# Kernel optimization log

Hardware: AMD Instinct MI355X
Metric: run time of the kernel (lower is better)

The kernel has to match this reference:

```python
import jax, jax.numpy as jnp
import numpy as np

D_MODEL = 1024
NUM_HEADS = 16
HEAD_DIM = D_MODEL // NUM_HEADS


def setup_inputs() -> dict:
    key = jax.random.key(0)
    ks = jax.random.split(key, 5)
    x = jax.random.normal(ks[0], (2, 2048, D_MODEL), dtype=jnp.float32)
    # torch nn.Linear init scale ~ U(-1/sqrt(in), 1/sqrt(in)); use small normals
    s = 1.0 / np.sqrt(D_MODEL)
    W_qkv = jax.random.normal(ks[1], (D_MODEL, 3 * D_MODEL), dtype=jnp.float32) * s
    b_qkv = jax.random.normal(ks[2], (3 * D_MODEL,), dtype=jnp.float32) * s
    W_out = jax.random.normal(ks[3], (D_MODEL, D_MODEL), dtype=jnp.float32) * s
    b_out = jax.random.normal(ks[4], (D_MODEL,), dtype=jnp.float32) * s
    return {"x": x, "W_qkv": W_qkv, "b_qkv": b_qkv, "W_out": W_out, "b_out": b_out}


def reference(x, W_qkv, b_qkv, W_out, b_out):
    B, S, _ = x.shape
    qkv = x @ W_qkv + b_qkv                                  # [B,S,3D]
    qkv = qkv.reshape(B, S, NUM_HEADS, 3 * HEAD_DIM).transpose(0, 2, 1, 3)  # [B,H,S,3d]
    q, k, v = jnp.split(qkv, 3, axis=-1)                     # each [B,H,S,d]
    scale = 1.0 / np.sqrt(HEAD_DIM)
    scores = jnp.einsum("bhqd,bhkd->bhqk", q, k) * scale      # [B,H,S,S]
    attn = jax.nn.softmax(scores, axis=-1)
    values = jnp.einsum("bhqk,bhkd->bhqd", attn, v)           # [B,H,S,d]
    values = values.transpose(0, 2, 1, 3).reshape(B, S, D_MODEL)
    return values @ W_out + b_out
```

## Files before the change

### kernel.cpp

```cpp
#include <hip/hip_runtime.h>


#define D_MODEL 1024
#define NHEAD   16
#define HDIM    64
#define SEQ     2048
#define BATCH   2
#define NTOK    (BATCH * SEQ)

typedef float    f32x4  __attribute__((ext_vector_type(4)));
typedef float    f32x16 __attribute__((ext_vector_type(16)));
typedef _Float16 f16x8  __attribute__((ext_vector_type(8)));
typedef _Float16 f16x4  __attribute__((ext_vector_type(4)));

#define GLOBAL_LOAD_LDS16(gptr, lptr)                                            \
    __builtin_amdgcn_global_load_lds(                                            \
        (const __attribute__((address_space(1))) unsigned int*)(gptr),           \
        (__attribute__((address_space(3))) unsigned int*)(lptr), 16, 0, 0)

__global__ __launch_bounds__(256) void prep_kernel(
    const float* __restrict__ x, _Float16* __restrict__ xh,
    const float* __restrict__ Wqkv, _Float16* __restrict__ wq_t,
    const float* __restrict__ Wout, _Float16* __restrict__ wo_t)
{
    const int bx = blockIdx.x;
    const int tid = threadIdx.x;
    if (bx < 4096) {
        const int i = (bx * 256 + tid) * 4;
        const float4 v = *(const float4*)&x[i];
        f16x4 hh;
        hh[0] = (_Float16)v.x; hh[1] = (_Float16)v.y;
        hh[2] = (_Float16)v.z; hh[3] = (_Float16)v.w;
        *(f16x4*)&xh[i] = hh;
        return;
    }
    __shared__ float ts[64][65];
    const float* W; _Float16* Wt; int N, n0, k0;
    if (bx < 4096 + 768) {
        const int local = bx - 4096;
        W = Wqkv; Wt = wq_t; N = 3072;
        n0 = (local % 48) * 64; k0 = (local / 48) * 64;
    } else {
        const int local = bx - 4864;
        W = Wout; Wt = wo_t; N = 1024;
        n0 = (local % 16) * 64; k0 = (local / 16) * 64;
    }
    {
        const int r = tid >> 2, c = (tid & 3) << 4;
        const float* src = W + (size_t)(k0 + r) * N + n0 + c;
        #pragma unroll
        for (int u = 0; u < 4; ++u)
            *(float4*)&ts[r][c + u * 4] = *(const float4*)&src[u * 4];
    }
    __syncthreads();
    {
        const int n = tid >> 2, kg = (tid & 3) << 4;
        f16x8 v0, v1;
        #pragma unroll
        for (int j = 0; j < 8; ++j) {
            v0[j] = (_Float16)ts[kg + j][n];
            v1[j] = (_Float16)ts[kg + 8 + j][n];
        }
        _Float16* dst = Wt + (size_t)(n0 + n) * D_MODEL + k0 + kg;
        *(f16x8*)&dst[0] = v0;
        *(f16x8*)&dst[8] = v1;
    }
}

__global__ __launch_bounds__(512) void gemm_qkv_kernel(
    const _Float16* __restrict__ A, const _Float16* __restrict__ Bt,
    const float* __restrict__ bias, _Float16* __restrict__ Cout,
    int M, int N, int K)
{
    __shared__ _Float16 lds[2][4096];
    const int tid = threadIdx.x;
    const int wave = tid >> 6, lane = tid & 63;
    const int quad = lane >> 4, l16 = lane & 15;
    const int m0 = blockIdx.y * 128, n0 = blockIdx.x * 128;
    const int wr = wave >> 1, wc = wave & 1;

    f32x4 acc[2][4] = {};

    const bool isA = wave < 4;
    const _Float16* gsrc = isA ? (A + (size_t)m0 * K) : (Bt + (size_t)n0 * K);
    _Float16* ldst = isA ? &lds[0][0] : &lds[1][0];
    const int sbase = (wave & 3) * 2;

    for (int k0 = 0; k0 < K; k0 += 32) {
        __syncthreads();
        #pragma unroll
        for (int j = 0; j < 2; ++j) {
            const int seg = sbase + j;
            const int chunk = seg >> 1;
            const int row = ((seg & 1) << 6) | lane;
            GLOBAL_LOAD_LDS16(gsrc + (size_t)row * K + k0 + chunk * 8, ldst + seg * 512);
        }
        __syncthreads();

        f16x8 a[2], b[4];
        #pragma unroll
        for (int mt = 0; mt < 2; ++mt)
            a[mt] = *(const f16x8*)&lds[0][quad * 1024 + (wr * 32 + mt * 16 + l16) * 8];
        #pragma unroll
        for (int nt = 0; nt < 4; ++nt)
            b[nt] = *(const f16x8*)&lds[1][quad * 1024 + (wc * 64 + nt * 16 + l16) * 8];
        #pragma unroll
        for (int mt = 0; mt < 2; ++mt)
            #pragma unroll
            for (int nt = 0; nt < 4; ++nt)
                acc[mt][nt] = __builtin_amdgcn_mfma_f32_16x16x32_f16(a[mt], b[nt], acc[mt][nt], 0, 0, 0);
    }

    #pragma unroll
    for (int nt = 0; nt < 4; ++nt) {
        const int col = n0 + wc * 64 + nt * 16 + l16;
        const float bv = bias[col];
        #pragma unroll
        for (int mt = 0; mt < 2; ++mt) {
            #pragma unroll
            for (int r = 0; r < 4; ++r) {
                const int row = m0 + wr * 32 + mt * 16 + quad * 4 + r;
                Cout[(size_t)row * N + col] = (_Float16)(acc[mt][nt][r] + bv);
            }
        }
    }
}

__global__ __launch_bounds__(512) void gemm_out_kernel(
    const _Float16* __restrict__ A, const _Float16* __restrict__ Bt,
    const float* __restrict__ bias, float* __restrict__ Cout)
{
    const int K = D_MODEL, N = D_MODEL;
    __shared__ _Float16 ldsA[4096];
    __shared__ _Float16 ldsB[2048];
    const int tid = threadIdx.x;
    const int wave = tid >> 6, lane = tid & 63;
    const int quad = lane >> 4, l16 = lane & 15;
    const int m0 = blockIdx.y * 128, n0 = blockIdx.x * 64;
    const int wr = wave >> 1, wc = wave & 1;

    f32x4 acc[2][2] = {};

    for (int k0 = 0; k0 < K; k0 += 32) {
        __syncthreads();
        if (wave < 4) {
            #pragma unroll
            for (int j = 0; j < 2; ++j) {
                const int seg = wave * 2 + j;
                const int chunk = seg >> 1;
                const int row = ((seg & 1) << 6) | lane;
                GLOBAL_LOAD_LDS16(A + (size_t)(m0 + row) * K + k0 + chunk * 8, ldsA + seg * 512);
            }
        } else {
            const int seg = wave - 4;
            GLOBAL_LOAD_LDS16(Bt + (size_t)(n0 + lane) * K + k0 + seg * 8, ldsB + seg * 512);
        }
        __syncthreads();

        f16x8 a[2], b[2];
        #pragma unroll
        for (int mt = 0; mt < 2; ++mt)
            a[mt] = *(const f16x8*)&ldsA[quad * 1024 + (wr * 32 + mt * 16 + l16) * 8];
        #pragma unroll
        for (int nt = 0; nt < 2; ++nt)
            b[nt] = *(const f16x8*)&ldsB[quad * 512 + (wc * 32 + nt * 16 + l16) * 8];
        #pragma unroll
        for (int mt = 0; mt < 2; ++mt)
            #pragma unroll
            for (int nt = 0; nt < 2; ++nt)
                acc[mt][nt] = __builtin_amdgcn_mfma_f32_16x16x32_f16(a[mt], b[nt], acc[mt][nt], 0, 0, 0);
    }

    #pragma unroll
    for (int nt = 0; nt < 2; ++nt) {
        const int col = n0 + wc * 32 + nt * 16 + l16;
        const float bv = bias[col];
        #pragma unroll
        for (int mt = 0; mt < 2; ++mt) {
            #pragma unroll
            for (int r = 0; r < 4; ++r) {
                const int row = m0 + wr * 32 + mt * 16 + quad * 4 + r;
                Cout[(size_t)row * N + col] = acc[mt][nt][r] + bv;
            }
        }
    }
}

__global__ __launch_bounds__(256) void swizzle_kv_kernel(
    const _Float16* __restrict__ qkv,
    _Float16* __restrict__ Ksw, _Float16* __restrict__ Vsw)
{
    __shared__ _Float16 ts[64][72];
    const int tid = threadIdx.x;
    const int s0 = blockIdx.x * 64, h = blockIdx.y, b = blockIdx.z;
    const size_t hsz = (size_t)8 * SEQ * 8;
    _Float16* kh = Ksw + (size_t)(b * NHEAD + h) * hsz;
    _Float16* vh = Vsw + (size_t)(b * NHEAD + h) * hsz;

    {
        const int s = s0 + (tid >> 2);
        const int dg = (tid & 3) << 4;
        const _Float16* src = qkv + (size_t)(b * SEQ + s) * (3 * D_MODEL) + h * (3 * HDIM) + HDIM + dg;
        const f16x8 v0 = *(const f16x8*)&src[0];
        const f16x8 v1 = *(const f16x8*)&src[8];
        const int c0 = dg >> 3;
        *(f16x8*)&kh[((size_t)c0 * SEQ + s) * 8]       = v0;
        *(f16x8*)&kh[((size_t)(c0 + 1) * SEQ + s) * 8] = v1;
    }
    {
        const int s = tid >> 2, dg = (tid & 3) << 4;
        const _Float16* src = qkv + (size_t)(b * SEQ + s0 + s) * (3 * D_MODEL) + h * (3 * HDIM) + 2 * HDIM + dg;
        *(f16x8*)&ts[s][dg]     = *(const f16x8*)&src[0];
        *(f16x8*)&ts[s][dg + 8] = *(const f16x8*)&src[8];
    }
    __syncthreads();
    {
        const int d = tid >> 2, sg = (tid & 3) << 4;
        f16x8 v0, v1;
        #pragma unroll
        for (int j = 0; j < 8; ++j) { v0[j] = ts[sg + j][d]; v1[j] = ts[sg + 8 + j][d]; }
        const int cs0 = (s0 + sg) >> 3;
        *(f16x8*)&vh[((size_t)cs0 * HDIM + d) * 8]       = v0;
        *(f16x8*)&vh[((size_t)(cs0 + 1) * HDIM + d) * 8] = v1;
    }
}

__device__ __forceinline__ void softmax_frag(
    const f32x16 s0, const f32x16 s1, float& rs, f16x8 pa[4])
{
    #pragma unroll
    for (int half = 0; half < 2; ++half) {
        const f32x16 sv = half ? s1 : s0;
        float p[16];
        #pragma unroll
        for (int r = 0; r < 16; ++r)
            p[r] = __builtin_amdgcn_exp2f(sv[r]);
        #pragma unroll
        for (int r = 0; r < 16; r += 4)
            rs += (p[r] + p[r + 1]) + (p[r + 2] + p[r + 3]);

        union { f16x8 hv; unsigned u[4]; } lo, hh;
        {
            const unsigned A = __builtin_bit_cast(unsigned, __builtin_amdgcn_cvt_pkrtz(p[0], p[1]));
            const unsigned B = __builtin_bit_cast(unsigned, __builtin_amdgcn_cvt_pkrtz(p[2], p[3]));
            const unsigned C = __builtin_bit_cast(unsigned, __builtin_amdgcn_cvt_pkrtz(p[4], p[5]));
            const unsigned D = __builtin_bit_cast(unsigned, __builtin_amdgcn_cvt_pkrtz(p[6], p[7]));
            const auto rac = __builtin_amdgcn_permlane32_swap(A, C, false, false);
            const auto rbd = __builtin_amdgcn_permlane32_swap(B, D, false, false);
            lo.u[0] = rac[0]; lo.u[1] = rbd[0]; lo.u[2] = rac[1]; lo.u[3] = rbd[1];
        }
        {
            const unsigned E = __builtin_bit_cast(unsigned, __builtin_amdgcn_cvt_pkrtz(p[8],  p[9]));
            const unsigned F = __builtin_bit_cast(unsigned, __builtin_amdgcn_cvt_pkrtz(p[10], p[11]));
            const unsigned G = __builtin_bit_cast(unsigned, __builtin_amdgcn_cvt_pkrtz(p[12], p[13]));
            const unsigned H = __builtin_bit_cast(unsigned, __builtin_amdgcn_cvt_pkrtz(p[14], p[15]));
            const auto reg = __builtin_amdgcn_permlane32_swap(E, G, false, false);
            const auto rfh = __builtin_amdgcn_permlane32_swap(F, H, false, false);
            hh.u[0] = reg[0]; hh.u[1] = rfh[0]; hh.u[2] = reg[1]; hh.u[3] = rfh[1];
        }
        pa[half * 2]     = lo.hv;
        pa[half * 2 + 1] = hh.hv;
    }
}

__global__ __launch_bounds__(512) void attn_mfma_kernel(
    const _Float16* __restrict__ qkv,
    const _Float16* __restrict__ Ksw, const _Float16* __restrict__ Vsw,
    _Float16* __restrict__ val)
{
    __shared__ _Float16 Ks[2][8192];
    __shared__ _Float16 Vts[2][8192];

    const int tid = threadIdx.x;
    const int wave = tid >> 6, lane = tid & 63;
    const int l31 = lane & 31, hi = lane >> 5;

    const int id = blockIdx.x;
    const int g  = (id & 7) * 32 + (id >> 3);
    const int qt = g & 7, hb = g >> 3;
    const int h  = hb & 15, b = hb >> 4;
    const int q0 = qt * 256;

    const size_t hsz = (size_t)8 * SEQ * 8;
    const _Float16* kh = Ksw + (size_t)(b * NHEAD + h) * hsz;
    const _Float16* vh = Vsw + (size_t)(b * NHEAD + h) * hsz;

    f16x8 qf[4];
    {
        const int row = q0 + wave * 32 + l31;
        const _Float16* src = qkv + (size_t)(b * SEQ + row) * (3 * D_MODEL) + h * (3 * HDIM) + hi * 8;
        #pragma unroll
        for (int kk = 0; kk < 4; ++kk) {
            const f16x8 t = *(const f16x8*)(src + kk * 16);
            #pragma unroll
            for (int j = 0; j < 8; ++j)
                qf[kk][j] = (_Float16)((float)t[j] * 0.1803368802f);
        }
    }

    f32x16 acc0 = {};
    f32x16 acc1 = {};
    float rs = 0.f;

    const int sidx0 = wave * 2;
    #pragma unroll
    for (int j = 0; j < 2; ++j) {
        const int idx = sidx0 + j;
        const int u = idx >> 3, c = idx & 7;
        GLOBAL_LOAD_LDS16(kh + ((size_t)c * SEQ + u * 64 + lane) * 8, &Ks[0][idx * 512]);
        GLOBAL_LOAD_LDS16(vh + ((size_t)(u * 8 + c) * HDIM + lane) * 8, &Vts[0][idx * 512]);
    }
    __syncthreads();

    for (int kt = 0; kt < SEQ / 128; ++kt) {
        const int cur = kt & 1;

        if (kt + 1 < SEQ / 128) {
            #pragma unroll
            for (int j = 0; j < 2; ++j) {
                const int idx = sidx0 + j;
                const int u = idx >> 3, c = idx & 7;
                GLOBAL_LOAD_LDS16(kh + ((size_t)c * SEQ + (kt + 1) * 128 + u * 64 + lane) * 8,
                                  &Ks[cur ^ 1][idx * 512]);
                GLOBAL_LOAD_LDS16(vh + ((size_t)((kt + 1) * 16 + u * 8 + c) * HDIM + lane) * 8,
                                  &Vts[cur ^ 1][idx * 512]);
            }
        }

        #pragma unroll
        for (int u = 0; u < 2; ++u) {
            const _Float16* ksub = &Ks[cur][u * 4096];
            const _Float16* vsub = &Vts[cur][u * 4096];

            f32x16 s0 = {}, s1 = {};
            __builtin_amdgcn_s_setprio(1);
            #pragma unroll
            for (int kk = 0; kk < 4; ++kk) {
                const f16x8 k0 = *(const f16x8*)&ksub[(kk * 2 + hi) * 512 + l31 * 8];
                const f16x8 k1 = *(const f16x8*)&ksub[(kk * 2 + hi) * 512 + (32 + l31) * 8];
                s0 = __builtin_amdgcn_mfma_f32_32x32x16_f16(k0, qf[kk], s0, 0, 0, 0);
                s1 = __builtin_amdgcn_mfma_f32_32x32x16_f16(k1, qf[kk], s1, 0, 0, 0);
            }
            __builtin_amdgcn_s_setprio(0);

            f16x8 pa[4];
            softmax_frag(s0, s1, rs, pa);

            __builtin_amdgcn_s_setprio(1);
            #pragma unroll
            for (int ks = 0; ks < 4; ++ks) {
                const f16x8 v0 = *(const f16x8*)&vsub[(ks * 2 + hi) * 512 + l31 * 8];
                const f16x8 v1 = *(const f16x8*)&vsub[(ks * 2 + hi) * 512 + (32 + l31) * 8];
                acc0 = __builtin_amdgcn_mfma_f32_32x32x16_f16(pa[ks], v0, acc0, 0, 0, 0);
                acc1 = __builtin_amdgcn_mfma_f32_32x32x16_f16(pa[ks], v1, acc1, 0, 0, 0);
            }
            __builtin_amdgcn_s_setprio(0);
        }

        __syncthreads();
    }

    rs += __shfl_xor(rs, 32);
    const float inv = 1.f / rs;

    #pragma unroll
    for (int r = 0; r < 16; ++r) {
        const int qo = (r & 3) + 8 * (r >> 2) + 4 * hi;
        const float invr = __shfl(inv, qo);
        const int row = b * SEQ + q0 + wave * 32 + qo;
        val[(size_t)row * D_MODEL + h * HDIM + l31]      = (_Float16)(acc0[r] * invr);
        val[(size_t)row * D_MODEL + h * HDIM + 32 + l31] = (_Float16)(acc1[r] * invr);
    }
}

extern "C" void kernel_launch(void* const* d_in, const int* in_sizes, int n_in,
                              void* d_out, int out_size, void* d_ws, size_t ws_size,
                              hipStream_t stream)
{
    const float* x     = (const float*)d_in[0];
    const float* W_qkv = (const float*)d_in[1];
    const float* b_qkv = (const float*)d_in[2];
    const float* W_out = (const float*)d_in[3];
    const float* b_out = (const float*)d_in[4];

    char* ws = (char*)d_ws;
    _Float16* Ksw   = (_Float16*)ws;
    _Float16* val_h = (_Float16*)(ws + (8u << 20));
    _Float16* wq_t  = (_Float16*)(ws + (16u << 20));
    _Float16* wo_t  = (_Float16*)(ws + (22u << 20));
    _Float16* qkv_h = (_Float16*)(ws + (24u << 20));
    _Float16* x_h   = (_Float16*)(ws + (48u << 20));
    _Float16* Vsw   = (_Float16*)(ws + (48u << 20));

    prep_kernel<<<5120, 256, 0, stream>>>(x, x_h, W_qkv, wq_t, W_out, wo_t);
    gemm_qkv_kernel<<<dim3(3 * D_MODEL / 128, NTOK / 128), 512, 0, stream>>>(
        x_h, wq_t, b_qkv, qkv_h, NTOK, 3 * D_MODEL, D_MODEL);
    swizzle_kv_kernel<<<dim3(SEQ / 64, NHEAD, BATCH), 256, 0, stream>>>(qkv_h, Ksw, Vsw);
    attn_mfma_kernel<<<dim3(256, 1, 1), 512, 0, stream>>>(qkv_h, Ksw, Vsw, val_h);
    gemm_out_kernel<<<dim3(D_MODEL / 64, NTOK / 128), 512, 0, stream>>>(
        val_h, wo_t, b_out, (float*)d_out);
}
```

Measured before the change: 216.6 us.

## Double-buffer LDS tiles in QKV and output projection GEMMs

Both projection GEMM kernels now keep two LDS buffers and issue the global-to-LDS loads for the next K tile before running the MFMAs on the current tile. This drops one barrier per iteration and is meant to overlap global memory latency with matrix math. It doubles LDS use per block, which may lower occupancy. Note that global_load_lds completion is only guaranteed by the vmcnt wait the compiler puts at the barrier, so correctness depends on that wait.

```diff
diff --git a/kernel.cpp b/kernel.cpp
--- a/kernel.cpp
+++ b/kernel.cpp
@@ -72,7 +72,7 @@
     const float* __restrict__ bias, _Float16* __restrict__ Cout,
     int M, int N, int K)
 {
-    __shared__ _Float16 lds[2][4096];
+    __shared__ _Float16 lds[2][2][4096];
     const int tid = threadIdx.x;
     const int wave = tid >> 6, lane = tid & 63;
     const int quad = lane >> 4, l16 = lane & 15;
@@ -83,32 +83,48 @@
 
     const bool isA = wave < 4;
     const _Float16* gsrc = isA ? (A + (size_t)m0 * K) : (Bt + (size_t)n0 * K);
-    _Float16* ldst = isA ? &lds[0][0] : &lds[1][0];
+    const int plane = isA ? 0 : 1;
     const int sbase = (wave & 3) * 2;
 
-    for (int k0 = 0; k0 < K; k0 += 32) {
-        __syncthreads();
-        #pragma unroll
-        for (int j = 0; j < 2; ++j) {
-            const int seg = sbase + j;
-            const int chunk = seg >> 1;
-            const int row = ((seg & 1) << 6) | lane;
-            GLOBAL_LOAD_LDS16(gsrc + (size_t)row * K + k0 + chunk * 8, ldst + seg * 512);
-        }
-        __syncthreads();
+    #pragma unroll
+    for (int j = 0; j < 2; ++j) {
+        const int seg = sbase + j;
+        const int chunk = seg >> 1;
+        const int row = ((seg & 1) << 6) | lane;
+        GLOBAL_LOAD_LDS16(gsrc + (size_t)row * K + chunk * 8, &lds[0][plane][seg * 512]);
+    }
+    __syncthreads();
+
+    const int nk = K / 32;
+    for (int t = 0; t < nk; ++t) {
+        const int cur = t & 1;
+
+        if (t + 1 < nk) {
+            const int k1 = (t + 1) * 32;
+            #pragma unroll
+            for (int j = 0; j < 2; ++j) {
+                const int seg = sbase + j;
+                const int chunk = seg >> 1;
+                const int row = ((seg & 1) << 6) | lane;
+                GLOBAL_LOAD_LDS16(gsrc + (size_t)row * K + k1 + chunk * 8,
+                                  &lds[cur ^ 1][plane][seg * 512]);
+            }
+        }
 
         f16x8 a[2], b[4];
         #pragma unroll
         for (int mt = 0; mt < 2; ++mt)
-            a[mt] = *(const f16x8*)&lds[0][quad * 1024 + (wr * 32 + mt * 16 + l16) * 8];
+            a[mt] = *(const f16x8*)&lds[cur][0][quad * 1024 + (wr * 32 + mt * 16 + l16) * 8];
         #pragma unroll
         for (int nt = 0; nt < 4; ++nt)
-            b[nt] = *(const f16x8*)&lds[1][quad * 1024 + (wc * 64 + nt * 16 + l16) * 8];
+            b[nt] = *(const f16x8*)&lds[cur][1][quad * 1024 + (wc * 64 + nt * 16 + l16) * 8];
         #pragma unroll
         for (int mt = 0; mt < 2; ++mt)
             #pragma unroll
             for (int nt = 0; nt < 4; ++nt)
                 acc[mt][nt] = __builtin_amdgcn_mfma_f32_16x16x32_f16(a[mt], b[nt], acc[mt][nt], 0, 0, 0);
+
+        __syncthreads();
     }
 
     #pragma unroll
@@ -131,8 +147,8 @@
     const float* __restrict__ bias, float* __restrict__ Cout)
 {
     const int K = D_MODEL, N = D_MODEL;
-    __shared__ _Float16 ldsA[4096];
-    __shared__ _Float16 ldsB[2048];
+    __shared__ _Float16 ldsA[2][4096];
+    __shared__ _Float16 ldsB[2][2048];
     const int tid = threadIdx.x;
     const int wave = tid >> 6, lane = tid & 63;
     const int quad = lane >> 4, l16 = lane & 15;
@@ -141,34 +157,56 @@
 
     f32x4 acc[2][2] = {};
 
-    for (int k0 = 0; k0 < K; k0 += 32) {
-        __syncthreads();
-        if (wave < 4) {
-            #pragma unroll
-            for (int j = 0; j < 2; ++j) {
-                const int seg = wave * 2 + j;
-                const int chunk = seg >> 1;
-                const int row = ((seg & 1) << 6) | lane;
-                GLOBAL_LOAD_LDS16(A + (size_t)(m0 + row) * K + k0 + chunk * 8, ldsA + seg * 512);
-            }
-        } else {
-            const int seg = wave - 4;
-            GLOBAL_LOAD_LDS16(Bt + (size_t)(n0 + lane) * K + k0 + seg * 8, ldsB + seg * 512);
-        }
-        __syncthreads();
+    if (wave < 4) {
+        #pragma unroll
+        for (int j = 0; j < 2; ++j) {
+            const int seg = wave * 2 + j;
+            const int chunk = seg >> 1;
+            const int row = ((seg & 1) << 6) | lane;
+            GLOBAL_LOAD_LDS16(A + (size_t)(m0 + row) * K + chunk * 8, &ldsA[0][seg * 512]);
+        }
+    } else {
+        const int seg = wave - 4;
+        GLOBAL_LOAD_LDS16(Bt + (size_t)(n0 + lane) * K + seg * 8, &ldsB[0][seg * 512]);
+    }
+    __syncthreads();
+
+    const int nk = K / 32;
+    for (int t = 0; t < nk; ++t) {
+        const int cur = t & 1;
+
+        if (t + 1 < nk) {
+            const int k1 = (t + 1) * 32;
+            if (wave < 4) {
+                #pragma unroll
+                for (int j = 0; j < 2; ++j) {
+                    const int seg = wave * 2 + j;
+                    const int chunk = seg >> 1;
+                    const int row = ((seg & 1) << 6) | lane;
+                    GLOBAL_LOAD_LDS16(A + (size_t)(m0 + row) * K + k1 + chunk * 8,
+                                      &ldsA[cur ^ 1][seg * 512]);
+                }
+            } else {
+                const int seg = wave - 4;
+                GLOBAL_LOAD_LDS16(Bt + (size_t)(n0 + lane) * K + k1 + seg * 8,
+                                  &ldsB[cur ^ 1][seg * 512]);
+            }
+        }
 
         f16x8 a[2], b[2];
         #pragma unroll
         for (int mt = 0; mt < 2; ++mt)
-            a[mt] = *(const f16x8*)&ldsA[quad * 1024 + (wr * 32 + mt * 16 + l16) * 8];
+            a[mt] = *(const f16x8*)&ldsA[cur][quad * 1024 + (wr * 32 + mt * 16 + l16) * 8];
         #pragma unroll
         for (int nt = 0; nt < 2; ++nt)
-            b[nt] = *(const f16x8*)&ldsB[quad * 512 + (wc * 32 + nt * 16 + l16) * 8];
+            b[nt] = *(const f16x8*)&ldsB[cur][quad * 512 + (wc * 32 + nt * 16 + l16) * 8];
         #pragma unroll
         for (int mt = 0; mt < 2; ++mt)
             #pragma unroll
             for (int nt = 0; nt < 2; ++nt)
                 acc[mt][nt] = __builtin_amdgcn_mfma_f32_16x16x32_f16(a[mt], b[nt], acc[mt][nt], 0, 0, 0);
+
+        __syncthreads();
     }
 
     #pragma unroll
```

New measurement: 216.8 us. No clear change (+0.1%).
